# Optimization experiments

Measured on AMD Instinct MI355X. Metric: run time of the kernel, lower is better.

Reference implementation:

```python
import jax, jax.numpy as jnp
import numpy as np

N, PAIR, M, D, O, R = 4096, 2, 64, 128, 128, 2
MAX_DEG = 32


def setup_inputs() -> dict:
    key = jax.random.key(0)
    k1, k2, k3, k4, k5, k6 = jax.random.split(key, 6)
    node_features = jax.random.normal(k1, (N, PAIR, M, D), dtype=jnp.float32)
    deg = jax.random.randint(k2, (N,), 0, MAX_DEG, dtype=jnp.int32)
    # per-relation Linear params (stored as [in, out]) and self-loop Linear
    W_r = jax.random.normal(k3, (R, D, O), dtype=jnp.float32) / np.sqrt(D)
    b_r = jax.random.normal(k4, (R, O), dtype=jnp.float32) * 0.01
    W0 = jax.random.normal(k5, (D, O), dtype=jnp.float32) / np.sqrt(D)
    b0 = jax.random.normal(k6, (O,), dtype=jnp.float32) * 0.01
    return {"node_features": node_features, "deg": deg, "W_r": W_r,
            "b_r": b_r, "W0": W0, "b0": b0}


def reference(node_features, deg, W_r, b_r, W0, b0):
    # Original: for each relation r, for each neighbor, adds W_r(x_i);
    # i.e. sum_r deg_i * (x_i @ W_r + b_r) = deg_i * (x_i @ sum_r W_r + sum_r b_r)
    Wsum = W_r.sum(axis=0)          # [D, O]
    bsum = b_r.sum(axis=0)          # [O]
    rel = jnp.einsum('npmd,do->npmo', node_features, Wsum) + bsum
    self_term = jnp.einsum('npmd,do->npmo', node_features, W0) + b0
    d = deg.astype(node_features.dtype)[:, None, None, None]
    h = jax.nn.relu(d * rel + self_term)  # [N, 2, M, O]
    # edge representation: mm(h_i, h_j.T) per entity -> [N, M, M]
    out = jnp.einsum('nmo,nko->nmk', h[:, 0], h[:, 1])
    return out
```

## Files before the change

### kernel.cpp

```cpp
#include <hip/hip_runtime.h>
#include <hip/hip_bf16.h>


typedef __attribute__((ext_vector_type(8))) short bf16x8;
typedef __attribute__((ext_vector_type(4))) float f32x4;

#define RAW_BARRIER() do {                                   \
    asm volatile("s_waitcnt lgkmcnt(0)" ::: "memory");       \
    __builtin_amdgcn_s_barrier();                            \
    __builtin_amdgcn_sched_barrier(0);                       \
} while (0)

__device__ __forceinline__ unsigned int pkbf(float a, float b) {
    union { __hip_bfloat162 h; unsigned int u; } v;
    v.h = __float22bfloat162_rn(float2{a, b});
    return v.u;
}

__global__ __launch_bounds__(256) void build_weights(
    const float* __restrict__ W_r,
    const float* __restrict__ b_r,
    const float* __restrict__ W0,
    const float* __restrict__ b0,
    unsigned short* __restrict__ wfrag,
    float* __restrict__ call)
{
    const int t = blockIdx.x * blockDim.x + threadIdx.x;
    const int d = t >> 11;
    const int r = t & 2047;
    const int k = r >> 4;
    const int o0 = (r & 15) * 8;
    const f32x4* wr0 = (const f32x4*)(W_r + k * 128 + o0);
    const f32x4* wr1 = (const f32x4*)(W_r + 128 * 128 + k * 128 + o0);
    const f32x4* w0p = (const f32x4*)(W0 + k * 128 + o0);
    float w[8];
#pragma unroll
    for (int half = 0; half < 2; ++half) {
        f32x4 a = wr0[half], b = wr1[half], c = w0p[half];
#pragma unroll
        for (int i = 0; i < 4; ++i)
            w[half * 4 + i] = (float)d * (a[i] + b[i]) + c[i];
    }
    const int ct = o0 >> 4;
    const int ks = k >> 5;
    const int lhi = (k >> 3) & 3;
    const int j = k & 7;
    unsigned short* base = wfrag +
        ((((size_t)(d * 8 + ct) * 4 + ks) * 64 + lhi * 16 + (o0 & 15))) * 8 + j;
#pragma unroll
    for (int i = 0; i < 8; ++i) {
        union { float f; unsigned u; } v; v.f = w[i];
        unsigned rr = (v.u + 0x7fffu + ((v.u >> 16) & 1u)) >> 16;
        base[i * 8] = (unsigned short)rr;
    }
    if (t < 32 * 128) {
        int dd = t >> 7, oo = t & 127;
        call[t] = (float)dd * (b_r[oo] + b_r[128 + oo]) + b0[oo];
    }
}

__global__ __launch_bounds__(256) void edge_kernel(
    const float* __restrict__ x,
    const int* __restrict__ deg,
    const unsigned short* __restrict__ wfrag,
    const float* __restrict__ call,
    float* __restrict__ out)
{
    __shared__ char ldsb[66048];

    const int n = blockIdx.x;
    const int tid = threadIdx.x;
    const int wave = tid >> 6;
    const int lane = tid & 63;
    const int l15 = lane & 15;
    const int lhi = lane >> 4;
    const int d = deg[n];

    const float* xn = x + (size_t)n * (2 * 64 * 128);
    const char* wsrc = (const char*)(wfrag + (size_t)d * (8 * 4 * 64 * 8));

#pragma unroll
    for (int i = 0; i < 8; ++i) {
        __builtin_amdgcn_global_load_lds(
            (const __attribute__((address_space(1))) unsigned int*)(wsrc + (size_t)i * 4096 + (size_t)tid * 16),
            (__attribute__((address_space(3))) unsigned int*)(ldsb + i * 4096 + wave * 1024),
            16, 0, 0);
    }
    if (tid < 32) {
        __builtin_amdgcn_global_load_lds(
            (const __attribute__((address_space(1))) unsigned int*)(call + d * 128 + tid * 4),
            (__attribute__((address_space(3))) unsigned int*)(ldsb + 65536),
            16, 0, 0);
    }

    const int rbase = wave * 32;
    const float* r0p = xn + (size_t)(rbase + l15) * 128 + lhi * 8;
    const float* r1p = r0p + (size_t)16 * 128;
    f32x4 xraw[2][4][2];
#pragma unroll
    for (int ks = 0; ks < 4; ++ks) {
        const f32x4* p0 = (const f32x4*)(r0p + ks * 32);
        const f32x4* p1 = (const f32x4*)(r1p + ks * 32);
        xraw[0][ks][0] = p0[0];
        xraw[0][ks][1] = p0[1];
        xraw[1][ks][0] = p1[0];
        xraw[1][ks][1] = p1[1];
    }
    bf16x8 afrag[2][4];
#pragma unroll
    for (int rt = 0; rt < 2; ++rt)
#pragma unroll
        for (int ks = 0; ks < 4; ++ks) {
            f32x4 a0 = xraw[rt][ks][0];
            f32x4 a1 = xraw[rt][ks][1];
            union { bf16x8 vv; unsigned int uu[4]; } f;
            f.uu[0] = pkbf(a0.x, a0.y);
            f.uu[1] = pkbf(a0.z, a0.w);
            f.uu[2] = pkbf(a1.x, a1.y);
            f.uu[3] = pkbf(a1.z, a1.w);
            afrag[rt][ks] = f.vv;
        }

    __syncthreads();

#pragma unroll
    for (int ct = 0; ct < 8; ++ct) {
        bf16x8 bfrag[4];
#pragma unroll
        for (int ks = 0; ks < 4; ++ks)
            bfrag[ks] = *(const bf16x8*)(ldsb + ct * 4096 + ks * 1024 + lane * 16);
        f32x4 acc[2] = {{0.f,0.f,0.f,0.f},{0.f,0.f,0.f,0.f}};
#pragma unroll
        for (int ks = 0; ks < 4; ++ks)
#pragma unroll
            for (int rt = 0; rt < 2; ++rt)
                acc[rt] = __builtin_amdgcn_mfma_f32_16x16x32_bf16(bfrag[ks], afrag[rt][ks], acc[rt], 0, 0, 0);
        const f32x4 cc4 = *(const f32x4*)(ldsb + 65536 + ct * 64 + lhi * 16);
#pragma unroll
        for (int rt = 0; rt < 2; ++rt) {
            const int m = rbase + rt * 16 + l15;
            const int slot = ((lhi >> 1) ^ ((m >> 2) & 1));
            float h0v = fmaxf(acc[rt][0] + cc4.x, 0.f);
            float h1v = fmaxf(acc[rt][1] + cc4.y, 0.f);
            float h2v = fmaxf(acc[rt][2] + cc4.z, 0.f);
            float h3v = fmaxf(acc[rt][3] + cc4.w, 0.f);
            union { unsigned int u[2]; unsigned long long ull; } pk;
            pk.u[0] = pkbf(h0v, h1v);
            pk.u[1] = pkbf(h2v, h3v);
            *(unsigned long long*)(ldsb + 32768 + ct * 4096 + m * 32 + slot * 16 + (lhi & 1) * 8) = pk.ull;
        }
    }
    RAW_BARRIER();

    const int mrow = wave * 16 + l15;
    bf16x8 hb[4];
#pragma unroll
    for (int ks = 0; ks < 4; ++ks) {
        const int ct = ks * 2 + (lhi >> 1);
        const int s  = (lhi & 1) ^ ((mrow >> 2) & 1);
        hb[ks] = *(const bf16x8*)(ldsb + 32768 + ct * 4096 + mrow * 32 + s * 16);
    }
    float* outn = out + (size_t)n * 4096;
#pragma unroll
    for (int qt = 0; qt < 4; ++qt) {
        const int qrow = 64 + qt * 16 + l15;
        f32x4 acc = {0.f, 0.f, 0.f, 0.f};
#pragma unroll
        for (int ks = 0; ks < 4; ++ks) {
            const int ct = ks * 2 + (lhi >> 1);
            const int s  = (lhi & 1) ^ ((qrow >> 2) & 1);
            bf16x8 ha = *(const bf16x8*)(ldsb + 32768 + ct * 4096 + qrow * 32 + s * 16);
            acc = __builtin_amdgcn_mfma_f32_16x16x32_bf16(ha, hb[ks], acc, 0, 0, 0);
        }
        __builtin_nontemporal_store(acc, (f32x4*)(outn + mrow * 64 + qt * 16 + lhi * 4));
    }
}

extern "C" void kernel_launch(void* const* d_in, const int* in_sizes, int n_in,
                              void* d_out, int out_size, void* d_ws, size_t ws_size,
                              hipStream_t stream) {
    const float* x   = (const float*)d_in[0];
    const int*   deg = (const int*)d_in[1];
    const float* W_r = (const float*)d_in[2];
    const float* b_r = (const float*)d_in[3];
    const float* W0  = (const float*)d_in[4];
    const float* b0  = (const float*)d_in[5];
    float* out = (float*)d_out;

    unsigned short* wfrag = (unsigned short*)d_ws;
    float* call = (float*)((unsigned short*)d_ws + 32 * 8 * 4 * 64 * 8);

    build_weights<<<256, 256, 0, stream>>>(W_r, b_r, W0, b0, wfrag, call);
    edge_kernel<<<4096, 256, 0, stream>>>(x, deg, wfrag, call, out);
}
```

Baseline: 69.56 us.

## Process two nodes per block and prefetch the second node during the first

Each workgroup now handles two consecutive nodes. The weight fragments and input rows for the second node are loaded into LDS and registers while the first node's output GEMM and stores run, which hides global load latency behind compute. The grid is halved to match. The cost is fewer blocks to spread across CUs and a longer-lived register set for the prefetched inputs.

```diff
diff --git a/kernel.cpp b/kernel.cpp
--- a/kernel.cpp
+++ b/kernel.cpp
@@ -68,111 +68,131 @@
 {
     __shared__ char ldsb[66048];
 
-    const int n = blockIdx.x;
     const int tid = threadIdx.x;
     const int wave = tid >> 6;
     const int lane = tid & 63;
     const int l15 = lane & 15;
     const int lhi = lane >> 4;
-    const int d = deg[n];
-
-    const float* xn = x + (size_t)n * (2 * 64 * 128);
-    const char* wsrc = (const char*)(wfrag + (size_t)d * (8 * 4 * 64 * 8));
-
-#pragma unroll
-    for (int i = 0; i < 8; ++i) {
-        __builtin_amdgcn_global_load_lds(
-            (const __attribute__((address_space(1))) unsigned int*)(wsrc + (size_t)i * 4096 + (size_t)tid * 16),
-            (__attribute__((address_space(3))) unsigned int*)(ldsb + i * 4096 + wave * 1024),
-            16, 0, 0);
-    }
-    if (tid < 32) {
-        __builtin_amdgcn_global_load_lds(
-            (const __attribute__((address_space(1))) unsigned int*)(call + d * 128 + tid * 4),
-            (__attribute__((address_space(3))) unsigned int*)(ldsb + 65536),
-            16, 0, 0);
-    }
-
     const int rbase = wave * 32;
-    const float* r0p = xn + (size_t)(rbase + l15) * 128 + lhi * 8;
-    const float* r1p = r0p + (size_t)16 * 128;
+    const int nb = blockIdx.x * 2;
+
+    const int d0 = deg[nb];
+    const int d1 = deg[nb + 1];
+
     f32x4 xraw[2][4][2];
-#pragma unroll
-    for (int ks = 0; ks < 4; ++ks) {
-        const f32x4* p0 = (const f32x4*)(r0p + ks * 32);
-        const f32x4* p1 = (const f32x4*)(r1p + ks * 32);
-        xraw[0][ks][0] = p0[0];
-        xraw[0][ks][1] = p0[1];
-        xraw[1][ks][0] = p1[0];
-        xraw[1][ks][1] = p1[1];
-    }
     bf16x8 afrag[2][4];
-#pragma unroll
-    for (int rt = 0; rt < 2; ++rt)
+
+    auto stage_w = [&](int d) {
+        const char* wsrc = (const char*)(wfrag + (size_t)d * (8 * 4 * 64 * 8));
+#pragma unroll
+        for (int i = 0; i < 8; ++i) {
+            __builtin_amdgcn_global_load_lds(
+                (const __attribute__((address_space(1))) unsigned int*)(wsrc + (size_t)i * 4096 + (size_t)tid * 16),
+                (__attribute__((address_space(3))) unsigned int*)(ldsb + i * 4096 + wave * 1024),
+                16, 0, 0);
+        }
+        if (tid < 32) {
+            __builtin_amdgcn_global_load_lds(
+                (const __attribute__((address_space(1))) unsigned int*)(call + d * 128 + tid * 4),
+                (__attribute__((address_space(3))) unsigned int*)(ldsb + 65536),
+                16, 0, 0);
+        }
+    };
+    auto issue_x = [&](int n) {
+        const float* r0p = x + (size_t)n * 16384 + (size_t)(rbase + l15) * 128 + lhi * 8;
 #pragma unroll
         for (int ks = 0; ks < 4; ++ks) {
-            f32x4 a0 = xraw[rt][ks][0];
-            f32x4 a1 = xraw[rt][ks][1];
-            union { bf16x8 vv; unsigned int uu[4]; } f;
-            f.uu[0] = pkbf(a0.x, a0.y);
-            f.uu[1] = pkbf(a0.z, a0.w);
-            f.uu[2] = pkbf(a1.x, a1.y);
-            f.uu[3] = pkbf(a1.z, a1.w);
-            afrag[rt][ks] = f.vv;
-        }
-
+            const f32x4* p0 = (const f32x4*)(r0p + ks * 32);
+            const f32x4* p1 = (const f32x4*)(r0p + 2048 + ks * 32);
+            xraw[0][ks][0] = p0[0];
+            xraw[0][ks][1] = p0[1];
+            xraw[1][ks][0] = p1[0];
+            xraw[1][ks][1] = p1[1];
+        }
+    };
+    auto convert_x = [&]() {
+#pragma unroll
+        for (int rt = 0; rt < 2; ++rt)
+#pragma unroll
+            for (int ks = 0; ks < 4; ++ks) {
+                f32x4 a0 = xraw[rt][ks][0];
+                f32x4 a1 = xraw[rt][ks][1];
+                union { bf16x8 vv; unsigned int uu[4]; } f;
+                f.uu[0] = pkbf(a0.x, a0.y);
+                f.uu[1] = pkbf(a0.z, a0.w);
+                f.uu[2] = pkbf(a1.x, a1.y);
+                f.uu[3] = pkbf(a1.z, a1.w);
+                afrag[rt][ks] = f.vv;
+            }
+    };
+
+    stage_w(d0);
+    issue_x(nb);
+    convert_x();
     __syncthreads();
 
-#pragma unroll
-    for (int ct = 0; ct < 8; ++ct) {
-        bf16x8 bfrag[4];
-#pragma unroll
-        for (int ks = 0; ks < 4; ++ks)
-            bfrag[ks] = *(const bf16x8*)(ldsb + ct * 4096 + ks * 1024 + lane * 16);
-        f32x4 acc[2] = {{0.f,0.f,0.f,0.f},{0.f,0.f,0.f,0.f}};
-#pragma unroll
-        for (int ks = 0; ks < 4; ++ks)
-#pragma unroll
-            for (int rt = 0; rt < 2; ++rt)
-                acc[rt] = __builtin_amdgcn_mfma_f32_16x16x32_bf16(bfrag[ks], afrag[rt][ks], acc[rt], 0, 0, 0);
-        const f32x4 cc4 = *(const f32x4*)(ldsb + 65536 + ct * 64 + lhi * 16);
-#pragma unroll
-        for (int rt = 0; rt < 2; ++rt) {
-            const int m = rbase + rt * 16 + l15;
-            const int slot = ((lhi >> 1) ^ ((m >> 2) & 1));
-            float h0v = fmaxf(acc[rt][0] + cc4.x, 0.f);
-            float h1v = fmaxf(acc[rt][1] + cc4.y, 0.f);
-            float h2v = fmaxf(acc[rt][2] + cc4.z, 0.f);
-            float h3v = fmaxf(acc[rt][3] + cc4.w, 0.f);
-            union { unsigned int u[2]; unsigned long long ull; } pk;
-            pk.u[0] = pkbf(h0v, h1v);
-            pk.u[1] = pkbf(h2v, h3v);
-            *(unsigned long long*)(ldsb + 32768 + ct * 4096 + m * 32 + slot * 16 + (lhi & 1) * 8) = pk.ull;
-        }
-    }
-    RAW_BARRIER();
-
-    const int mrow = wave * 16 + l15;
-    bf16x8 hb[4];
-#pragma unroll
-    for (int ks = 0; ks < 4; ++ks) {
-        const int ct = ks * 2 + (lhi >> 1);
-        const int s  = (lhi & 1) ^ ((mrow >> 2) & 1);
-        hb[ks] = *(const bf16x8*)(ldsb + 32768 + ct * 4096 + mrow * 32 + s * 16);
-    }
-    float* outn = out + (size_t)n * 4096;
-#pragma unroll
-    for (int qt = 0; qt < 4; ++qt) {
-        const int qrow = 64 + qt * 16 + l15;
-        f32x4 acc = {0.f, 0.f, 0.f, 0.f};
+    for (int j = 0; j < 2; ++j) {
+#pragma unroll
+        for (int ct = 0; ct < 8; ++ct) {
+            bf16x8 bfrag[4];
+#pragma unroll
+            for (int ks = 0; ks < 4; ++ks)
+                bfrag[ks] = *(const bf16x8*)(ldsb + ct * 4096 + ks * 1024 + lane * 16);
+            f32x4 acc[2] = {{0.f,0.f,0.f,0.f},{0.f,0.f,0.f,0.f}};
+#pragma unroll
+            for (int ks = 0; ks < 4; ++ks)
+#pragma unroll
+                for (int rt = 0; rt < 2; ++rt)
+                    acc[rt] = __builtin_amdgcn_mfma_f32_16x16x32_bf16(bfrag[ks], afrag[rt][ks], acc[rt], 0, 0, 0);
+            const f32x4 cc4 = *(const f32x4*)(ldsb + 65536 + ct * 64 + lhi * 16);
+#pragma unroll
+            for (int rt = 0; rt < 2; ++rt) {
+                const int m = rbase + rt * 16 + l15;
+                const int slot = ((lhi >> 1) ^ ((m >> 2) & 1));
+                float h0v = fmaxf(acc[rt][0] + cc4.x, 0.f);
+                float h1v = fmaxf(acc[rt][1] + cc4.y, 0.f);
+                float h2v = fmaxf(acc[rt][2] + cc4.z, 0.f);
+                float h3v = fmaxf(acc[rt][3] + cc4.w, 0.f);
+                union { unsigned int u[2]; unsigned long long ull; } pk;
+                pk.u[0] = pkbf(h0v, h1v);
+                pk.u[1] = pkbf(h2v, h3v);
+                *(unsigned long long*)(ldsb + 32768 + ct * 4096 + m * 32 + slot * 16 + (lhi & 1) * 8) = pk.ull;
+            }
+        }
+        RAW_BARRIER();
+
+        if (j == 0) {
+            stage_w(d1);
+            issue_x(nb + 1);
+        }
+
+        const int mrow = wave * 16 + l15;
+        bf16x8 hb[4];
 #pragma unroll
         for (int ks = 0; ks < 4; ++ks) {
             const int ct = ks * 2 + (lhi >> 1);
-            const int s  = (lhi & 1) ^ ((qrow >> 2) & 1);
-            bf16x8 ha = *(const bf16x8*)(ldsb + 32768 + ct * 4096 + qrow * 32 + s * 16);
-            acc = __builtin_amdgcn_mfma_f32_16x16x32_bf16(ha, hb[ks], acc, 0, 0, 0);
-        }
-        __builtin_nontemporal_store(acc, (f32x4*)(outn + mrow * 64 + qt * 16 + lhi * 4));
+            const int s  = (lhi & 1) ^ ((mrow >> 2) & 1);
+            hb[ks] = *(const bf16x8*)(ldsb + 32768 + ct * 4096 + mrow * 32 + s * 16);
+        }
+        float* outn = out + (size_t)(nb + j) * 4096;
+#pragma unroll
+        for (int qt = 0; qt < 4; ++qt) {
+            const int qrow = 64 + qt * 16 + l15;
+            f32x4 acc = {0.f, 0.f, 0.f, 0.f};
+#pragma unroll
+            for (int ks = 0; ks < 4; ++ks) {
+                const int ct = ks * 2 + (lhi >> 1);
+                const int s  = (lhi & 1) ^ ((qrow >> 2) & 1);
+                bf16x8 ha = *(const bf16x8*)(ldsb + 32768 + ct * 4096 + qrow * 32 + s * 16);
+                acc = __builtin_amdgcn_mfma_f32_16x16x32_bf16(ha, hb[ks], acc, 0, 0, 0);
+            }
+            __builtin_nontemporal_store(acc, (f32x4*)(outn + mrow * 64 + qt * 16 + lhi * 4));
+        }
+
+        if (j == 0) {
+            convert_x();
+            __syncthreads();
+        }
     }
 }
 
@@ -191,5 +211,5 @@
     float* call = (float*)((unsigned short*)d_ws + 32 * 8 * 4 * 64 * 8);
 
     build_weights<<<256, 256, 0, stream>>>(W_r, b_r, W0, b0, wfrag, call);
-    edge_kernel<<<4096, 256, 0, stream>>>(x, deg, wfrag, call, out);
-}
+    edge_kernel<<<2048, 256, 0, stream>>>(x, deg, wfrag, call, out);
+}
```

New measurement: 73.16 us. 5.2% more time.

## Double edge_kernel block to 512 threads, splitting rows and output tiles per wave

Applied to the files above, without the earlier changes.

Launches edge_kernel with 512 threads (8 waves) per node instead of 256. In the first GEMM each wave now handles 16 rows instead of 32. In the second GEMM each wave computes two output tiles instead of four. The weight-fragment LDS load is redistributed over the larger block. This aims to raise latency hiding and per-block parallelism, at the cost of more waves per block, which with 66KB of LDS per block may limit residency and adds barrier cost.

```diff
diff --git a/kernel.cpp b/kernel.cpp
--- a/kernel.cpp
+++ b/kernel.cpp
@@ -59,7 +59,7 @@
     }
 }
 
-__global__ __launch_bounds__(256) void edge_kernel(
+__global__ __launch_bounds__(512) void edge_kernel(
     const float* __restrict__ x,
     const int* __restrict__ deg,
     const unsigned short* __restrict__ wfrag,
@@ -80,10 +80,10 @@
     const char* wsrc = (const char*)(wfrag + (size_t)d * (8 * 4 * 64 * 8));
 
 #pragma unroll
-    for (int i = 0; i < 8; ++i) {
+    for (int i = 0; i < 4; ++i) {
         __builtin_amdgcn_global_load_lds(
-            (const __attribute__((address_space(1))) unsigned int*)(wsrc + (size_t)i * 4096 + (size_t)tid * 16),
-            (__attribute__((address_space(3))) unsigned int*)(ldsb + i * 4096 + wave * 1024),
+            (const __attribute__((address_space(1))) unsigned int*)(wsrc + (size_t)i * 8192 + (size_t)tid * 16),
+            (__attribute__((address_space(3))) unsigned int*)(ldsb + i * 8192 + wave * 1024),
             16, 0, 0);
     }
     if (tid < 32) {
@@ -93,33 +93,26 @@
             16, 0, 0);
     }
 
-    const int rbase = wave * 32;
-    const float* r0p = xn + (size_t)(rbase + l15) * 128 + lhi * 8;
-    const float* r1p = r0p + (size_t)16 * 128;
-    f32x4 xraw[2][4][2];
+    const float* r0p = xn + (size_t)(wave * 16 + l15) * 128 + lhi * 8;
+    f32x4 xraw[4][2];
 #pragma unroll
     for (int ks = 0; ks < 4; ++ks) {
         const f32x4* p0 = (const f32x4*)(r0p + ks * 32);
-        const f32x4* p1 = (const f32x4*)(r1p + ks * 32);
-        xraw[0][ks][0] = p0[0];
-        xraw[0][ks][1] = p0[1];
-        xraw[1][ks][0] = p1[0];
-        xraw[1][ks][1] = p1[1];
+        xraw[ks][0] = p0[0];
+        xraw[ks][1] = p0[1];
     }
-    bf16x8 afrag[2][4];
+    bf16x8 afrag[4];
 #pragma unroll
-    for (int rt = 0; rt < 2; ++rt)
-#pragma unroll
-        for (int ks = 0; ks < 4; ++ks) {
-            f32x4 a0 = xraw[rt][ks][0];
-            f32x4 a1 = xraw[rt][ks][1];
-            union { bf16x8 vv; unsigned int uu[4]; } f;
-            f.uu[0] = pkbf(a0.x, a0.y);
-            f.uu[1] = pkbf(a0.z, a0.w);
-            f.uu[2] = pkbf(a1.x, a1.y);
-            f.uu[3] = pkbf(a1.z, a1.w);
-            afrag[rt][ks] = f.vv;
-        }
+    for (int ks = 0; ks < 4; ++ks) {
+        f32x4 a0 = xraw[ks][0];
+        f32x4 a1 = xraw[ks][1];
+        union { bf16x8 vv; unsigned int uu[4]; } f;
+        f.uu[0] = pkbf(a0.x, a0.y);
+        f.uu[1] = pkbf(a0.z, a0.w);
+        f.uu[2] = pkbf(a1.x, a1.y);
+        f.uu[3] = pkbf(a1.z, a1.w);
+        afrag[ks] = f.vv;
+    }
 
     __syncthreads();
 
@@ -129,30 +122,25 @@
 #pragma unroll
         for (int ks = 0; ks < 4; ++ks)
             bfrag[ks] = *(const bf16x8*)(ldsb + ct * 4096 + ks * 1024 + lane * 16);
-        f32x4 acc[2] = {{0.f,0.f,0.f,0.f},{0.f,0.f,0.f,0.f}};
+        f32x4 acc = {0.f, 0.f, 0.f, 0.f};
 #pragma unroll
         for (int ks = 0; ks < 4; ++ks)
-#pragma unroll
-            for (int rt = 0; rt < 2; ++rt)
-                acc[rt] = __builtin_amdgcn_mfma_f32_16x16x32_bf16(bfrag[ks], afrag[rt][ks], acc[rt], 0, 0, 0);
+            acc = __builtin_amdgcn_mfma_f32_16x16x32_bf16(bfrag[ks], afrag[ks], acc, 0, 0, 0);
         const f32x4 cc4 = *(const f32x4*)(ldsb + 65536 + ct * 64 + lhi * 16);
-#pragma unroll
-        for (int rt = 0; rt < 2; ++rt) {
-            const int m = rbase + rt * 16 + l15;
-            const int slot = ((lhi >> 1) ^ ((m >> 2) & 1));
-            float h0v = fmaxf(acc[rt][0] + cc4.x, 0.f);
-            float h1v = fmaxf(acc[rt][1] + cc4.y, 0.f);
-            float h2v = fmaxf(acc[rt][2] + cc4.z, 0.f);
-            float h3v = fmaxf(acc[rt][3] + cc4.w, 0.f);
-            union { unsigned int u[2]; unsigned long long ull; } pk;
-            pk.u[0] = pkbf(h0v, h1v);
-            pk.u[1] = pkbf(h2v, h3v);
-            *(unsigned long long*)(ldsb + 32768 + ct * 4096 + m * 32 + slot * 16 + (lhi & 1) * 8) = pk.ull;
-        }
+        const int m = wave * 16 + l15;
+        const int slot = ((lhi >> 1) ^ ((m >> 2) & 1));
+        float h0v = fmaxf(acc[0] + cc4.x, 0.f);
+        float h1v = fmaxf(acc[1] + cc4.y, 0.f);
+        float h2v = fmaxf(acc[2] + cc4.z, 0.f);
+        float h3v = fmaxf(acc[3] + cc4.w, 0.f);
+        union { unsigned int u[2]; unsigned long long ull; } pk;
+        pk.u[0] = pkbf(h0v, h1v);
+        pk.u[1] = pkbf(h2v, h3v);
+        *(unsigned long long*)(ldsb + 32768 + ct * 4096 + m * 32 + slot * 16 + (lhi & 1) * 8) = pk.ull;
     }
     RAW_BARRIER();
 
-    const int mrow = wave * 16 + l15;
+    const int mrow = (wave >> 1) * 16 + l15;
     bf16x8 hb[4];
 #pragma unroll
     for (int ks = 0; ks < 4; ++ks) {
@@ -162,7 +150,8 @@
     }
     float* outn = out + (size_t)n * 4096;
 #pragma unroll
-    for (int qt = 0; qt < 4; ++qt) {
+    for (int q = 0; q < 2; ++q) {
+        const int qt = (wave & 1) * 2 + q;
         const int qrow = 64 + qt * 16 + l15;
         f32x4 acc = {0.f, 0.f, 0.f, 0.f};
 #pragma unroll
@@ -191,5 +180,5 @@
     float* call = (float*)((unsigned short*)d_ws + 32 * 8 * 4 * 64 * 8);
 
     build_weights<<<256, 256, 0, stream>>>(W_r, b_r, W0, b0, wfrag, call);
-    edge_kernel<<<4096, 256, 0, stream>>>(x, deg, wfrag, call, out);
+    edge_kernel<<<4096, 512, 0, stream>>>(x, deg, wfrag, call, out);
 }
```

New measurement: 69.39 us. Within noise of the previous version (-0.2%).
